# Optimization experiments

Measured on AMD Instinct MI355X. Metric: run time of the kernel, lower is better.

The kernel has to match this reference:

```python
import jax, jax.numpy as jnp
import numpy as np

EMBED_DIM = 768
NUM_HEADS = 12
HEAD_DIM = EMBED_DIM // NUM_HEADS


def setup_inputs() -> dict:
    key = jax.random.key(0)
    k1, k2, k3 = jax.random.split(key, 3)
    B, T = 128, 128
    x = jax.random.normal(k1, (B, T, EMBED_DIM), dtype=jnp.float32)
    # weights stored as [in, out] so forward is x @ W (equivalent to torch Linear, bias=False)
    w_qkv = jax.random.normal(k2, (EMBED_DIM, 3 * EMBED_DIM), dtype=jnp.float32) * (EMBED_DIM ** -0.5)
    w_proj = jax.random.normal(k3, (EMBED_DIM, EMBED_DIM), dtype=jnp.float32) * (EMBED_DIM ** -0.5)
    return {"x": x, "w_qkv": w_qkv, "w_proj": w_proj}


def reference(x, w_qkv, w_proj):
    B, T, C = x.shape
    # fused QKV projection -> (3, B, H, T, D)
    qkv = (x @ w_qkv).reshape(B, T, 3, NUM_HEADS, HEAD_DIM)
    q, k, v = jnp.transpose(qkv, (2, 0, 3, 1, 4))
    # scaled dot-product scores (B, H, T, T)
    att = jnp.einsum('bhqd,bhkd->bhqk', q, k) * (HEAD_DIM ** -0.5)
    causal = jnp.tril(jnp.ones((T, T), dtype=bool))
    att = jnp.where(causal, att, -jnp.inf)
    # float32 softmax then cast back (matches att.float().softmax().to(x.dtype))
    att = jax.nn.softmax(att.astype(jnp.float32), axis=-1).astype(x.dtype)
    # dropout is identity in eval/reference mode
    out = jnp.einsum('bhqk,bhkd->bhqd', att, v)          # (B, H, T, D)
    out = jnp.transpose(out, (0, 2, 1, 3)).reshape(B, T, C)
    return out @ w_proj
```

## Files before the change

### kernel.cpp

```cpp
#include <hip/hip_runtime.h>

typedef __bf16 bf16_t;
typedef bf16_t bf16x8 __attribute__((ext_vector_type(8)));
typedef bf16_t bf16x4 __attribute__((ext_vector_type(4)));
typedef float f32x4 __attribute__((ext_vector_type(4)));

__device__ __forceinline__ f32x4 mfma16(bf16x8 a, bf16x8 b, f32x4 c) {
  return __builtin_amdgcn_mfma_f32_16x16x32_bf16(a, b, c, 0, 0, 0);
}

__device__ __forceinline__ void gload16(const bf16_t* g, bf16_t* l) {
  __builtin_amdgcn_global_load_lds(
      (const __attribute__((address_space(1))) void*)g,
      (__attribute__((address_space(3))) void*)l, 16, 0, 0);
}

__global__ void prep_kernel(const float* __restrict__ x, const float* __restrict__ wq,
                            const float* __restrict__ wp, bf16_t* __restrict__ xb,
                            bf16_t* __restrict__ wqt, bf16_t* __restrict__ wpt) {
  __shared__ bf16_t tile[32][33];
  const int bid = blockIdx.x;
  if (bid < 12288) {
    int i = bid * 256 + threadIdx.x;
    float4 v = ((const float4*)x)[i];
    bf16x4 o;
    o[0] = (bf16_t)v.x; o[1] = (bf16_t)v.y; o[2] = (bf16_t)v.z; o[3] = (bf16_t)v.w;
    *(bf16x4*)&xb[(size_t)i * 4] = o;
    return;
  }
  const int t = bid - 12288;
  const int ty = t / 96, txb = t % 96;
  const float* in;
  bf16_t* out;
  int N, n0;
  if (txb < 72) { in = wq; out = wqt; N = 2304; n0 = txb * 32; }
  else          { in = wp; out = wpt; N = 768;  n0 = (txb - 72) * 32; }
  const int k0 = ty * 32;
  const int tx = threadIdx.x & 31, tyy = threadIdx.x >> 5;
#pragma unroll
  for (int ph = 0; ph < 4; ++ph) {
    int k = tyy + ph * 8;
    tile[k][tx] = (bf16_t)in[(size_t)(k0 + k) * N + n0 + tx];
  }
  __syncthreads();
#pragma unroll
  for (int ph = 0; ph < 4; ++ph) {
    int n = tyy + ph * 8;
    out[(size_t)(n0 + n) * 768 + k0 + tx] = tile[tx][n];
  }
}

template <int BN, bool F32OUT>
__global__ __launch_bounds__(256, 3) void gemm_persist(
    const bf16_t* __restrict__ A, const bf16_t* __restrict__ Bt,
    void* __restrict__ Cout, int N, int K, int nbn, int q, int r) {
  constexpr int NQ = BN / 32;
  __shared__ bf16_t As[2][128 * 64];
  __shared__ bf16_t Bs[2][BN * 64];
  const int tid = threadIdx.x;
  const int lane = tid & 63;
  const int w = tid >> 6;
  const int wm = w >> 1, wn = w & 1;
  const int lr = lane & 15, kg = lane >> 4;

  const int G = gridDim.x;
  const int bid = blockIdx.x;
  const int lb = (bid & 7) * (G >> 3) + (bid >> 3);
  int nj, start;
  if (lb < r) { nj = q + 1; start = lb * (q + 1); }
  else        { nj = q;     start = r * (q + 1) + (lb - r) * q; }

  const int NKT = K >> 6;
  const int sr = tid >> 3, sslot = tid & 7;

  auto stage = [&](int buf, const bf16_t* Aj, const bf16_t* Bj, int k0) {
#pragma unroll
    for (int it = 0; it < 4; ++it) {
      int rr = it * 32 + sr;
      gload16(Aj + (size_t)rr * K + (k0 + ((sslot ^ (rr & 7)) << 3)),
              &As[buf][(it * 256 + tid) * 8]);
    }
#pragma unroll
    for (int it = 0; it < NQ; ++it) {
      int rr = it * 32 + sr;
      gload16(Bj + (size_t)rr * K + (k0 + ((sslot ^ (rr & 7)) << 3)),
              &Bs[buf][(it * 256 + tid) * 8]);
    }
  };

  int job = start;
  int bm = job / nbn, bn = job % nbn;
  const bf16_t* Aj = A + (size_t)bm * 128 * K;
  const bf16_t* Bj = Bt + (size_t)bn * BN * K;
  stage(0, Aj, Bj, 0);
  __syncthreads();
  int buf = 0;

  for (int j = 0; j < nj; ++j) {
    f32x4 acc[4][NQ];
#pragma unroll
    for (int i = 0; i < 4; ++i)
#pragma unroll
      for (int n = 0; n < NQ; ++n) acc[i][n] = (f32x4){0.f, 0.f, 0.f, 0.f};

    int nbm = 0, nbnx = 0;
    const bf16_t *nAj = nullptr, *nBj = nullptr;
    if (j + 1 < nj) {
      int njob = job + 1;
      nbm = njob / nbn; nbnx = njob % nbn;
      nAj = A + (size_t)nbm * 128 * K;
      nBj = Bt + (size_t)nbnx * BN * K;
    }

    for (int kt = 0; kt < NKT; ++kt) {
      if (kt + 1 < NKT)      stage(buf ^ 1, Aj, Bj, (kt + 1) << 6);
      else if (j + 1 < nj)   stage(buf ^ 1, nAj, nBj, 0);
#pragma unroll
      for (int kk = 0; kk < 2; ++kk) {
        const int slot = ((kk << 2) + kg) ^ (lr & 7);
        bf16x8 af[4], bfv[NQ];
#pragma unroll
        for (int mq = 0; mq < 4; ++mq) {
          int rr = wm * 64 + mq * 16 + lr;
          af[mq] = *(const bf16x8*)&As[buf][(rr << 6) + (slot << 3)];
        }
#pragma unroll
        for (int nq = 0; nq < NQ; ++nq) {
          int rr = wn * (BN / 2) + nq * 16 + lr;
          bfv[nq] = *(const bf16x8*)&Bs[buf][(rr << 6) + (slot << 3)];
        }
#pragma unroll
        for (int mq = 0; mq < 4; ++mq)
#pragma unroll
          for (int nq = 0; nq < NQ; ++nq)
            acc[mq][nq] = mfma16(af[mq], bfv[nq], acc[mq][nq]);
      }
      __syncthreads();
      buf ^= 1;
    }

    const int row0 = bm * 128 + wm * 64 + kg * 4;
    const int col0 = bn * BN + wn * (BN / 2) + lr;
#pragma unroll
    for (int mq = 0; mq < 4; ++mq)
#pragma unroll
      for (int nq = 0; nq < NQ; ++nq)
#pragma unroll
        for (int rr = 0; rr < 4; ++rr) {
          size_t idx = (size_t)(row0 + mq * 16 + rr) * N + (col0 + nq * 16);
          if constexpr (F32OUT)
            ((float*)Cout)[idx] = acc[mq][nq][rr];
          else
            ((bf16_t*)Cout)[idx] = (bf16_t)acc[mq][nq][rr];
        }

    job++; bm = nbm; bn = nbnx; Aj = nAj; Bj = nBj;
  }
}

#define ATT_H 12
__global__ __launch_bounds__(256, 2) void attn_kernel(const bf16_t* __restrict__ qkv,
                                                      bf16_t* __restrict__ obuf) {
  __shared__ bf16_t Ks[128 * 72];
  __shared__ bf16_t Vt[64 * 136];
  __shared__ bf16_t Ps[128 * 136];
  const int tid = threadIdx.x, lane = tid & 63, w = tid >> 6;
  const int lr = lane & 15, kg = lane >> 4;
  const int bh = blockIdx.x;
  const int b = bh / ATT_H, h = bh % ATT_H;
  const size_t base = (size_t)b * 128 * 2304;
  const int hoff = h * 64;

#pragma unroll
  for (int it = 0; it < 4; ++it) {
    int idx = it * 256 + tid;
    int r = idx >> 3, slot = idx & 7;
    bf16x8 v = *(const bf16x8*)&qkv[base + (size_t)r * 2304 + 768 + hoff + slot * 8];
    *(bf16x8*)&Ks[r * 72 + slot * 8] = v;
  }
#pragma unroll 4
  for (int it = 0; it < 32; ++it) {
    int idx = it * 256 + tid;
    int t = idx >> 6, d = idx & 63;
    Vt[d * 136 + t] = qkv[base + (size_t)t * 2304 + 1536 + hoff + d];
  }
  const int qrow0 = w * 32;
  bf16x8 qf[2][2];
#pragma unroll
  for (int mt = 0; mt < 2; ++mt)
#pragma unroll
    for (int kk = 0; kk < 2; ++kk)
      qf[mt][kk] = *(const bf16x8*)&qkv[base + (size_t)(qrow0 + mt * 16 + lr) * 2304 + hoff +
                                        kk * 32 + kg * 8];
  __syncthreads();

  const int NT = 2 * w + 2;
  f32x4 acc[2][8];
#pragma unroll
  for (int mt = 0; mt < 2; ++mt)
#pragma unroll
    for (int nt = 0; nt < 8; ++nt) acc[mt][nt] = (f32x4){0.f, 0.f, 0.f, 0.f};

#pragma unroll
  for (int nt = 0; nt < 8; ++nt) {
    if (nt < NT) {
#pragma unroll
      for (int kk = 0; kk < 2; ++kk) {
        bf16x8 kf = *(const bf16x8*)&Ks[(nt * 16 + lr) * 72 + kk * 32 + kg * 8];
        acc[0][nt] = mfma16(qf[0][kk], kf, acc[0][nt]);
        acc[1][nt] = mfma16(qf[1][kk], kf, acc[1][nt]);
      }
    }
  }

#pragma unroll
  for (int mt = 0; mt < 2; ++mt) {
#pragma unroll
    for (int rr = 0; rr < 4; ++rr) {
      const int row = qrow0 + mt * 16 + kg * 4 + rr;
      float m = -1e30f;
#pragma unroll
      for (int nt = 0; nt < 8; ++nt) {
        if (nt < NT) {
          int col = nt * 16 + lr;
          float s = acc[mt][nt][rr] * 0.125f;
          s = (col <= row) ? s : -1e30f;
          acc[mt][nt][rr] = s;
          m = fmaxf(m, s);
        }
      }
      m = fmaxf(m, __shfl_xor(m, 1));
      m = fmaxf(m, __shfl_xor(m, 2));
      m = fmaxf(m, __shfl_xor(m, 4));
      m = fmaxf(m, __shfl_xor(m, 8));
      float ssum = 0.f;
#pragma unroll
      for (int nt = 0; nt < 8; ++nt) {
        if (nt < NT) {
          float p = __builtin_amdgcn_exp2f((acc[mt][nt][rr] - m) * 1.44269504f);
          acc[mt][nt][rr] = p;
          ssum += p;
        }
      }
      ssum += __shfl_xor(ssum, 1);
      ssum += __shfl_xor(ssum, 2);
      ssum += __shfl_xor(ssum, 4);
      ssum += __shfl_xor(ssum, 8);
      float inv = 1.0f / ssum;
#pragma unroll
      for (int nt = 0; nt < 8; ++nt) {
        if (nt < NT) Ps[row * 136 + nt * 16 + lr] = (bf16_t)(acc[mt][nt][rr] * inv);
      }
    }
  }

  f32x4 oacc[2][4];
#pragma unroll
  for (int mt = 0; mt < 2; ++mt)
#pragma unroll
    for (int dt = 0; dt < 4; ++dt) oacc[mt][dt] = (f32x4){0.f, 0.f, 0.f, 0.f};

  const int KS = w + 1;
#pragma unroll
  for (int ks = 0; ks < 4; ++ks) {
    if (ks < KS) {
      bf16x8 pa0 = *(const bf16x8*)&Ps[(qrow0 + lr) * 136 + ks * 32 + kg * 8];
      bf16x8 pa1 = *(const bf16x8*)&Ps[(qrow0 + 16 + lr) * 136 + ks * 32 + kg * 8];
#pragma unroll
      for (int dt = 0; dt < 4; ++dt) {
        bf16x8 vb = *(const bf16x8*)&Vt[(dt * 16 + lr) * 136 + ks * 32 + kg * 8];
        oacc[0][dt] = mfma16(pa0, vb, oacc[0][dt]);
        oacc[1][dt] = mfma16(pa1, vb, oacc[1][dt]);
      }
    }
  }

#pragma unroll
  for (int mt = 0; mt < 2; ++mt)
#pragma unroll
    for (int dt = 0; dt < 4; ++dt)
#pragma unroll
      for (int rr = 0; rr < 4; ++rr) {
        int t = qrow0 + mt * 16 + kg * 4 + rr;
        obuf[((size_t)b * 128 + t) * 768 + hoff + dt * 16 + lr] = (bf16_t)oacc[mt][dt][rr];
      }
}

extern "C" void kernel_launch(void* const* d_in, const int* in_sizes, int n_in,
                              void* d_out, int out_size, void* d_ws, size_t ws_size,
                              hipStream_t stream) {
  const float* x = (const float*)d_in[0];
  const float* w_qkv = (const float*)d_in[1];
  const float* w_proj = (const float*)d_in[2];
  float* out = (float*)d_out;
  char* ws = (char*)d_ws;

  bf16_t* xb     = (bf16_t*)(ws);
  bf16_t* wqkvt  = (bf16_t*)(ws + 25165824);
  bf16_t* wprojt = (bf16_t*)(ws + 28704768);
  bf16_t* qkv    = (bf16_t*)(ws + 29884416);
  bf16_t* obuf   = (bf16_t*)(ws + 105381888);

  prep_kernel<<<dim3(12288 + 2304), dim3(256), 0, stream>>>(x, w_qkv, w_proj, xb, wqkvt, wprojt);
  gemm_persist<128, false><<<dim3(512), dim3(256), 0, stream>>>(
      xb, wqkvt, (void*)qkv, 2304, 768, 18, 4, 256);
  attn_kernel<<<dim3(1536), dim3(256), 0, stream>>>(qkv, obuf);
  gemm_persist<64, true><<<dim3(768), dim3(256), 0, stream>>>(
      obuf, wprojt, (void*)out, 768, 768, 12, 2, 0);
}
```

Measured before the change: 157.9 us.

## Load GEMM B operand directly into registers and reassign persistent jobs per block

Replaces the persistent GEMM with a variant in which only the A tile is staged through LDS. The B (weight) fragments are loaded straight from global memory into registers, double-buffered across k-steps. Each block handles a fixed run of jobs that share one A row-block, and the output projection now uses 128-wide N tiles, one job per block. This removes LDS traffic and space for B and lets A be reused across consecutive N tiles, at the cost of more register pressure and uncoalesced global loads for B.

```diff
diff --git a/kernel.cpp b/kernel.cpp
--- a/kernel.cpp
+++ b/kernel.cpp
@@ -50,13 +50,13 @@
   }
 }
 
-template <int BN, bool F32OUT>
-__global__ __launch_bounds__(256, 3) void gemm_persist(
+template <int NBN, int JPB, bool F32OUT>
+__global__ __launch_bounds__(256, 3) void gemm_bl(
     const bf16_t* __restrict__ A, const bf16_t* __restrict__ Bt,
-    void* __restrict__ Cout, int N, int K, int nbn, int q, int r) {
-  constexpr int NQ = BN / 32;
+    void* __restrict__ Cout, int N) {
+  constexpr int K = 768;
+  constexpr int NKT = 12;
   __shared__ bf16_t As[2][128 * 64];
-  __shared__ bf16_t Bs[2][BN * 64];
   const int tid = threadIdx.x;
   const int lane = tid & 63;
   const int w = tid >> 6;
@@ -66,85 +66,88 @@
   const int G = gridDim.x;
   const int bid = blockIdx.x;
   const int lb = (bid & 7) * (G >> 3) + (bid >> 3);
-  int nj, start;
-  if (lb < r) { nj = q + 1; start = lb * (q + 1); }
-  else        { nj = q;     start = r * (q + 1) + (lb - r) * q; }
-
-  const int NKT = K >> 6;
+  const int start = lb * JPB;
+  const int bm = start / NBN;
+  const int bn0 = start - bm * NBN;
+  const bf16_t* Aj = A + (size_t)bm * (128 * K);
+
   const int sr = tid >> 3, sslot = tid & 7;
-
-  auto stage = [&](int buf, const bf16_t* Aj, const bf16_t* Bj, int k0) {
+  auto stageA = [&](int buf, int k0) {
 #pragma unroll
     for (int it = 0; it < 4; ++it) {
       int rr = it * 32 + sr;
       gload16(Aj + (size_t)rr * K + (k0 + ((sslot ^ (rr & 7)) << 3)),
               &As[buf][(it * 256 + tid) * 8]);
     }
-#pragma unroll
-    for (int it = 0; it < NQ; ++it) {
-      int rr = it * 32 + sr;
-      gload16(Bj + (size_t)rr * K + (k0 + ((sslot ^ (rr & 7)) << 3)),
-              &Bs[buf][(it * 256 + tid) * 8]);
-    }
   };
 
-  int job = start;
-  int bm = job / nbn, bn = job % nbn;
-  const bf16_t* Aj = A + (size_t)bm * 128 * K;
-  const bf16_t* Bj = Bt + (size_t)bn * BN * K;
-  stage(0, Aj, Bj, 0);
+  auto loadB = [&](bf16x8 (&dst)[4][2], int bn, int kt) {
+    const size_t rb = (size_t)(bn * 128 + wn * 64 + lr) * K + (kt << 6) + kg * 8;
+#pragma unroll
+    for (int nq = 0; nq < 4; ++nq)
+#pragma unroll
+      for (int kk = 0; kk < 2; ++kk)
+        dst[nq][kk] = *(const bf16x8*)&Bt[rb + (size_t)nq * (16 * K) + kk * 32];
+  };
+
+  f32x4 acc[4][4];
+  bf16x8 BA[4][2], BB[4][2];
+
+  auto compute = [&](int buf, bf16x8 (&B)[4][2]) {
+#pragma unroll
+    for (int kk = 0; kk < 2; ++kk) {
+      const int slot = ((kk << 2) + kg) ^ (lr & 7);
+      bf16x8 af[4];
+#pragma unroll
+      for (int mq = 0; mq < 4; ++mq) {
+        int rr = wm * 64 + mq * 16 + lr;
+        af[mq] = *(const bf16x8*)&As[buf][(rr << 6) + (slot << 3)];
+      }
+#pragma unroll
+      for (int mq = 0; mq < 4; ++mq)
+#pragma unroll
+        for (int nq = 0; nq < 4; ++nq)
+          acc[mq][nq] = mfma16(af[mq], B[nq][kk], acc[mq][nq]);
+    }
+  };
+
+  stageA(0, 0);
+  loadB(BA, bn0, 0);
   __syncthreads();
   int buf = 0;
 
-  for (int j = 0; j < nj; ++j) {
-    f32x4 acc[4][NQ];
+  for (int j = 0; j < JPB; ++j) {
+    const int bn = bn0 + j;
 #pragma unroll
     for (int i = 0; i < 4; ++i)
 #pragma unroll
-      for (int n = 0; n < NQ; ++n) acc[i][n] = (f32x4){0.f, 0.f, 0.f, 0.f};
-
-    int nbm = 0, nbnx = 0;
-    const bf16_t *nAj = nullptr, *nBj = nullptr;
-    if (j + 1 < nj) {
-      int njob = job + 1;
-      nbm = njob / nbn; nbnx = njob % nbn;
-      nAj = A + (size_t)nbm * 128 * K;
-      nBj = Bt + (size_t)nbnx * BN * K;
-    }
-
-    for (int kt = 0; kt < NKT; ++kt) {
-      if (kt + 1 < NKT)      stage(buf ^ 1, Aj, Bj, (kt + 1) << 6);
-      else if (j + 1 < nj)   stage(buf ^ 1, nAj, nBj, 0);
-#pragma unroll
-      for (int kk = 0; kk < 2; ++kk) {
-        const int slot = ((kk << 2) + kg) ^ (lr & 7);
-        bf16x8 af[4], bfv[NQ];
-#pragma unroll
-        for (int mq = 0; mq < 4; ++mq) {
-          int rr = wm * 64 + mq * 16 + lr;
-          af[mq] = *(const bf16x8*)&As[buf][(rr << 6) + (slot << 3)];
-        }
-#pragma unroll
-        for (int nq = 0; nq < NQ; ++nq) {
-          int rr = wn * (BN / 2) + nq * 16 + lr;
-          bfv[nq] = *(const bf16x8*)&Bs[buf][(rr << 6) + (slot << 3)];
-        }
-#pragma unroll
-        for (int mq = 0; mq < 4; ++mq)
-#pragma unroll
-          for (int nq = 0; nq < NQ; ++nq)
-            acc[mq][nq] = mfma16(af[mq], bfv[nq], acc[mq][nq]);
-      }
+      for (int n = 0; n < 4; ++n) acc[i][n] = (f32x4){0.f, 0.f, 0.f, 0.f};
+
+    for (int kt2 = 0; kt2 < NKT / 2; ++kt2) {
+      const int kt = kt2 * 2;
+      stageA(buf ^ 1, (kt + 1) << 6);
+      loadB(BB, bn, kt + 1);
+      compute(buf, BA);
       __syncthreads();
       buf ^= 1;
+      const bool injob = (kt + 2 < NKT);
+      const bool haveNext = injob || (j + 1 < JPB);
+      if (haveNext) {
+        const int nk = injob ? kt + 2 : 0;
+        stageA(buf ^ 1, nk << 6);
+        loadB(BA, injob ? bn : bn + 1, nk);
+      }
+      compute(buf, BB);
+      __syncthreads();
+      buf ^= 1;
     }
 
     const int row0 = bm * 128 + wm * 64 + kg * 4;
-    const int col0 = bn * BN + wn * (BN / 2) + lr;
+    const int col0 = bn * 128 + wn * 64 + lr;
 #pragma unroll
     for (int mq = 0; mq < 4; ++mq)
 #pragma unroll
-      for (int nq = 0; nq < NQ; ++nq)
+      for (int nq = 0; nq < 4; ++nq)
 #pragma unroll
         for (int rr = 0; rr < 4; ++rr) {
           size_t idx = (size_t)(row0 + mq * 16 + rr) * N + (col0 + nq * 16);
@@ -153,8 +156,6 @@
           else
             ((bf16_t*)Cout)[idx] = (bf16_t)acc[mq][nq][rr];
         }
-
-    job++; bm = nbm; bn = nbnx; Aj = nAj; Bj = nBj;
   }
 }
 
@@ -223,10 +224,10 @@
       for (int nt = 0; nt < 8; ++nt) {
         if (nt < NT) {
           int col = nt * 16 + lr;
-          float s = acc[mt][nt][rr] * 0.125f;
-          s = (col <= row) ? s : -1e30f;
-          acc[mt][nt][rr] = s;
-          m = fmaxf(m, s);
+          float sv = acc[mt][nt][rr] * 0.125f;
+          sv = (col <= row) ? sv : -1e30f;
+          acc[mt][nt][rr] = sv;
+          m = fmaxf(m, sv);
         }
       }
       m = fmaxf(m, __shfl_xor(m, 1));
@@ -302,9 +303,7 @@
   bf16_t* obuf   = (bf16_t*)(ws + 105381888);
 
   prep_kernel<<<dim3(12288 + 2304), dim3(256), 0, stream>>>(x, w_qkv, w_proj, xb, wqkvt, wprojt);
-  gemm_persist<128, false><<<dim3(512), dim3(256), 0, stream>>>(
-      xb, wqkvt, (void*)qkv, 2304, 768, 18, 4, 256);
+  gemm_bl<18, 3, false><<<dim3(768), dim3(256), 0, stream>>>(xb, wqkvt, (void*)qkv, 2304);
   attn_kernel<<<dim3(1536), dim3(256), 0, stream>>>(qkv, obuf);
-  gemm_persist<64, true><<<dim3(768), dim3(256), 0, stream>>>(
-      obuf, wprojt, (void*)out, 768, 768, 12, 2, 0);
-}
+  gemm_bl<6, 1, true><<<dim3(768), dim3(256), 0, stream>>>(obuf, wprojt, (void*)out, 768);
+}
```

New measurement: 243.3 us. +54.1%, slower.
